# Kernel tuning notes

Hardware: AMD Instinct MI355X
Metric: run time of the kernel (lower is better)

Reference implementation:

```python
import jax, jax.numpy as jnp
import numpy as np

USER_NUM, ITEM_NUM, EMB, R = 8192, 16384, 32, 3

def setup_inputs() -> dict:
    key = jax.random.key(0)
    k1, k2, k3 = jax.random.split(key, 3)
    # Xavier-uniform-like embeddings
    u_lim = (6.0 / (USER_NUM + EMB)) ** 0.5
    i_lim = (6.0 / (ITEM_NUM + EMB)) ** 0.5
    user_emb = jax.random.uniform(k1, (USER_NUM, EMB), jnp.float32, -u_lim, u_lim)
    item_emb = jax.random.uniform(k2, (ITEM_NUM, EMB), jnp.float32, -i_lim, i_lim)
    # Densified normalized link-propagation matrix (user x item).
    # Scale ~1/item_num so repeated propagation stays numerically tame,
    # mimicking the degree-normalized product in __init__.
    sparse_norm = jax.random.uniform(k3, (USER_NUM, ITEM_NUM), jnp.float32) * (2.0 / ITEM_NUM)
    return {"user_emb": user_emb, "item_emb": item_emb, "sparse_norm": sparse_norm}

def reference(user_emb, item_emb, sparse_norm):
    # LinkProp forward (t == 0.0 branch): r rounds of cross propagation,
    # then mean over the (r+1) layer outputs. Running sums avoid stacking.
    u_k, i_k = user_emb, item_emb
    u_sum, i_sum = user_emb, item_emb
    for _ in range(R):
        u_next = sparse_norm @ i_k          # [U, d]
        i_next = sparse_norm.T @ u_k        # [I, d]
        u_sum = u_sum + u_next
        i_sum = i_sum + i_next
        u_k, i_k = u_next, i_next
    inv = 1.0 / (R + 1)
    return (u_sum * inv, i_sum * inv)
```

## Files before the change

kernel.cpp:

```cpp
#include <hip/hip_runtime.h>

#define U_N 8192
#define I_N 16384

typedef float f4 __attribute__((ext_vector_type(4)));
typedef unsigned long long u64;
typedef unsigned char u8;

#if defined(__has_builtin)
#if __has_builtin(__builtin_amdgcn_cvt_pk_fp8_f32)
#define HAS_HW_FP8 1
#endif
#endif
#ifndef HAS_HW_FP8
#define HAS_HW_FP8 0
#endif

__device__ __forceinline__ unsigned char f2e4m3_soft(float x) {
  unsigned char sign = (x < 0.f) ? 0x80 : 0x00;
  float ax = fabsf(x);
  unsigned char code;
  if (ax >= 448.f) {
    code = 0x7E;
  } else if (ax < 0.015625f) {
    int q = (int)rintf(ax * 512.f);
    code = (unsigned char)q;
  } else {
    int e; float f = frexpf(ax, &e);
    int q = (int)rintf(f * 16.f);
    if (q == 16) { q = 8; e += 1; }
    code = (unsigned char)(((e + 6) << 3) | (q - 8));
  }
  return sign | code;
}

__device__ __forceinline__ unsigned char q8(float x) {
#if HAS_HW_FP8
  return (unsigned char)(__builtin_amdgcn_cvt_pk_fp8_f32(x, 0.f, 0, false) & 0xff);
#else
  return f2e4m3_soft(x);
#endif
}

__device__ __forceinline__ unsigned int pack4_fp8(float a, float b, float c, float d) {
#if HAS_HW_FP8
  int v = __builtin_amdgcn_cvt_pk_fp8_f32(a, b, 0, false);
  v = __builtin_amdgcn_cvt_pk_fp8_f32(c, d, v, true);
  return (unsigned int)v;
#else
  return (unsigned)f2e4m3_soft(a) | ((unsigned)f2e4m3_soft(b) << 8) |
         ((unsigned)f2e4m3_soft(c) << 16) | ((unsigned)f2e4m3_soft(d) << 24);
#endif
}

#define SCALE_S   131072.f
#define SCALE_V0  512.f
#define SCALE_VK  65536.f

__global__ __launch_bounds__(256)
void convert_kernel(const float* __restrict__ Sf,
                    const float* __restrict__ u0,
                    const float* __restrict__ i0,
                    u8* __restrict__ S8,
                    u8* __restrict__ S8T,
                    u8* __restrict__ wT0,
                    u8* __restrict__ vT0)
{
  const int tid = threadIdx.x;
  const int bid = blockIdx.x;
  if (bid < 1024) {
    const int idx = bid * 256 + tid;
    wT0[(size_t)(idx & 31) * U_N + (idx >> 5)] = q8(u0[idx] * SCALE_V0);
  } else if (bid < 3072) {
    const int idx = (bid - 1024) * 256 + tid;
    vT0[(size_t)(idx & 31) * I_N + (idx >> 5)] = q8(i0[idx] * SCALE_V0);
  } else {
    __shared__ unsigned char lds[64 * 68];
    const int b = bid - 3072;
    const int tr = b >> 8;
    const int tc = b & 255;
    const int mr = (tid >> 4) << 2;
    const int mc = (tid & 15) << 2;
    const size_t base = ((size_t)tr * 64 + mr) * I_N + (size_t)tc * 64 + mc;
    float fs[4][4];
#pragma unroll
    for (int i = 0; i < 4; ++i) {
      float4 f = *(const float4*)(Sf + base + (size_t)i * I_N);
      fs[i][0] = f.x * SCALE_S; fs[i][1] = f.y * SCALE_S;
      fs[i][2] = f.z * SCALE_S; fs[i][3] = f.w * SCALE_S;
    }
#pragma unroll
    for (int i = 0; i < 4; ++i)
      *(unsigned int*)&S8[base + (size_t)i * I_N] =
          pack4_fp8(fs[i][0], fs[i][1], fs[i][2], fs[i][3]);
#pragma unroll
    for (int j = 0; j < 4; ++j)
      *(unsigned int*)&lds[(mc + j) * 68 + mr] =
          pack4_fp8(fs[0][j], fs[1][j], fs[2][j], fs[3][j]);
    __syncthreads();
    const int c = tid >> 2;
    const int s = (tid & 3) << 4;
    uint4 v;
    v.x = *(const unsigned int*)&lds[c * 68 + s];
    v.y = *(const unsigned int*)&lds[c * 68 + s + 4];
    v.z = *(const unsigned int*)&lds[c * 68 + s + 8];
    v.w = *(const unsigned int*)&lds[c * 68 + s + 12];
    *(uint4*)&S8T[((size_t)tc * 64 + c) * U_N + (size_t)tr * 64 + s] = v;
  }
}

union B16 { uint4 v; long l[2]; };

template <int NE>
__global__ __launch_bounds__(256, 4)
void sweep_kernel(const u8* __restrict__ A, const u8* __restrict__ Bt,
                  float* __restrict__ part, int rg_mask, int rg_shift,
                  int nrows, int kdim, float ds_lo, float ds_hi)
{
  __shared__ u8 smem[NE * 528];
  const int tid = threadIdx.x;
  const int lane = tid & 63, wave = tid >> 6;
  const int m = lane & 15, quad = lane >> 4;
  const int bid = blockIdx.x;
  const int rgroup = bid & rg_mask, ksplit = bid >> rg_shift;
  const int r0 = rgroup * 64 + wave * 16;
  const int kbase = ksplit * 2048;
  f4 acc[NE / 16];
#pragma unroll
  for (int eb = 0; eb < NE / 16; ++eb) acc[eb] = {0.f, 0.f, 0.f, 0.f};

  const u8* arow = A + (size_t)(r0 + m) * kdim;

  for (int ch = 0; ch < 4; ++ch) {
    const int kb = kbase + ch * 512;
#pragma unroll
    for (int it = 0; it < NE / 8; ++it) {
      const int idx = it * 256 + tid;
      const int e = idx >> 5;
      const int o = (idx & 31) * 16;
      *(uint4*)&smem[e * 528 + o] = *(const uint4*)&Bt[(size_t)e * kdim + kb + o];
    }
    __syncthreads();
#pragma unroll
    for (int pr = 0; pr < 8; ++pr) {
      B16 av;
      av.v = *(const uint4*)(arow + kb + pr * 64 + quad * 16);
#pragma unroll
      for (int eb = 0; eb < NE / 16; ++eb) {
        B16 bv;
        bv.v = *(const uint4*)&smem[(m + eb * 16) * 528 + pr * 64 + quad * 16];
        acc[eb] = __builtin_amdgcn_mfma_f32_16x16x32_fp8_fp8(av.l[0], bv.l[0], acc[eb], 0, 0, 0);
        acc[eb] = __builtin_amdgcn_mfma_f32_16x16x32_fp8_fp8(av.l[1], bv.l[1], acc[eb], 0, 0, 0);
      }
    }
    __syncthreads();
  }
  float* dst = part + (size_t)ksplit * ((size_t)nrows * NE);
#pragma unroll
  for (int eb = 0; eb < NE / 16; ++eb) {
    const float ds = (eb < 2) ? ds_lo : ds_hi;
#pragma unroll
    for (int i2 = 0; i2 < 4; ++i2) {
      const int r = r0 + quad * 4 + i2;
      dst[(size_t)r * NE + eb * 16 + m] = acc[eb][i2] * ds;
    }
  }
}

__global__ __launch_bounds__(256)
void reduce_uA(const float* __restrict__ u_part, const float* __restrict__ u0,
               float* __restrict__ acc_u, u8* __restrict__ wT64)
{
  const int gid = blockIdx.x * 256 + threadIdx.x;
  float s = 0.f;
#pragma unroll
  for (int sp = 0; sp < 8; ++sp) s += u_part[(size_t)sp * (U_N * 32) + gid];
  acc_u[gid] = u0[gid] + s;
  wT64[(size_t)(32 + (gid & 31)) * U_N + (gid >> 5)] = q8(s * SCALE_VK);
}

__global__ __launch_bounds__(256)
void reduce_iB(const float* __restrict__ i_part, const float* __restrict__ i0,
               float* __restrict__ acc_i, u8* __restrict__ vT64)
{
  const int gid = blockIdx.x * 256 + threadIdx.x;
  const int c = gid >> 5, e = gid & 31;
  float s1 = 0.f, s2 = 0.f;
#pragma unroll
  for (int sp = 0; sp < 4; ++sp) {
    s1 += i_part[(size_t)sp * (I_N * 64) + (size_t)c * 64 + e];
    s2 += i_part[(size_t)sp * (I_N * 64) + (size_t)c * 64 + 32 + e];
  }
  acc_i[gid] = i0[gid] + s1 + s2;
  vT64[(size_t)e * I_N + c]        = q8(s1 * SCALE_VK);
  vT64[(size_t)(32 + e) * I_N + c] = q8(s2 * SCALE_VK);
}

__global__ __launch_bounds__(256)
void reduce_uC(const float* __restrict__ u_part, const float* __restrict__ acc_u,
               float* __restrict__ out_u, u8* __restrict__ wT2)
{
  const int gid = blockIdx.x * 256 + threadIdx.x;
  const int r = gid >> 5, e = gid & 31;
  float s2 = 0.f, s3 = 0.f;
#pragma unroll
  for (int sp = 0; sp < 8; ++sp) {
    s2 += u_part[(size_t)sp * (U_N * 64) + (size_t)r * 64 + e];
    s3 += u_part[(size_t)sp * (U_N * 64) + (size_t)r * 64 + 32 + e];
  }
  out_u[gid] = (acc_u[gid] + s2 + s3) * 0.25f;
  wT2[(size_t)e * U_N + r] = q8(s2 * SCALE_VK);
}

__global__ __launch_bounds__(256)
void reduce_iD(const float* __restrict__ i_part, const float* __restrict__ acc_i,
               float* __restrict__ out_i)
{
  const int gid = blockIdx.x * 256 + threadIdx.x;
  float s = 0.f;
#pragma unroll
  for (int sp = 0; sp < 4; ++sp) s += i_part[(size_t)sp * (I_N * 32) + gid];
  out_i[gid] = (acc_i[gid] + s) * 0.25f;
}

__global__ __launch_bounds__(256, 4)
void pass_fallback(const float* __restrict__ Sf,
                   const u8* __restrict__ vT,
                   const u8* __restrict__ wT,
                   float* __restrict__ u_part,
                   float* __restrict__ i_part,
                   float descale)
{
  __shared__ unsigned char smem[16896];
  const int tid = threadIdx.x;
  const int lane = tid & 63;
  const int wave = tid >> 6;
  const int m = lane & 15;
  const int quad = lane >> 4;
  const int bid = blockIdx.x;

  if (bid < 1024) {
    const int rg = bid & 127, ks = bid >> 7;
    const int r0 = rg * 64 + wave * 16;
    const int cbase = ks * 2048;
    f4 acc0 = {0.f, 0.f, 0.f, 0.f};
    f4 acc1 = {0.f, 0.f, 0.f, 0.f};
    for (int ch = 0; ch < 4; ++ch) {
      const int cb = cbase + ch * 512;
#pragma unroll
      for (int it = 0; it < 4; ++it) {
        const int idx = it * 256 + tid;
        const int e = idx >> 5;
        const int o = (idx & 31) * 16;
        *(uint4*)&smem[e * 528 + o] = *(const uint4*)&vT[(size_t)e * I_N + cb + o];
      }
      __syncthreads();
#pragma unroll
      for (int kk = 0; kk < 512; kk += 32) {
        const float* p = Sf + (size_t)(r0 + m) * I_N + cb + kk + quad * 8;
        u64 av = 0;
#pragma unroll
        for (int j = 0; j < 8; ++j) av |= (u64)q8(p[j] * SCALE_S) << (8 * j);
        const long a = (long)av;
        const long b0 = *(const long*)&smem[m * 528 + kk + quad * 8];
        const long b1 = *(const long*)&smem[(m + 16) * 528 + kk + quad * 8];
        acc0 = __builtin_amdgcn_mfma_f32_16x16x32_fp8_fp8(a, b0, acc0, 0, 0, 0);
        acc1 = __builtin_amdgcn_mfma_f32_16x16x32_fp8_fp8(a, b1, acc1, 0, 0, 0);
      }
      __syncthreads();
    }
    float* dst = u_part + (size_t)ks * (U_N * 32);
#pragma unroll
    for (int i2 = 0; i2 < 4; ++i2) {
      const int r = r0 + quad * 4 + i2;
      dst[r * 32 + m]      = acc0[i2] * descale;
      dst[r * 32 + 16 + m] = acc1[i2] * descale;
    }
  } else {
    const int b = bid - 1024;
    const int cg = b & 255, rs = b >> 8;
    const int c0 = cg * 64;
    const int rbase = rs * 2048;
    const int cw = wave * 16;
    unsigned char* stile = smem;
    unsigned char* wlds  = smem + 9216;
    f4 acc0 = {0.f, 0.f, 0.f, 0.f};
    f4 acc1 = {0.f, 0.f, 0.f, 0.f};
    for (int ch = 0; ch < 16; ++ch) {
      const int rb = rbase + ch * 128;
#pragma unroll
      for (int it = 0; it < 4; ++it) {
        const int idx = it * 256 + tid;
        const int rr = idx >> 3;
        const int o = (idx & 7) * 8;
        const float* p = Sf + (size_t)(rb + rr) * I_N + c0 + o;
        u64 v = 0;
#pragma unroll
        for (int j = 0; j < 8; ++j) v |= (u64)q8(p[j] * SCALE_S) << (8 * j);
        *(u64*)&stile[rr * 72 + o] = v;
      }
      {
        const int e = tid >> 3;
        const int o = (tid & 7) * 16;
        *(uint4*)&wlds[e * 144 + o] = *(const uint4*)&wT[(size_t)e * U_N + rb + o];
      }
      __syncthreads();
#pragma unroll
      for (int kk = 0; kk < 128; kk += 32) {
        u64 av = 0;
#pragma unroll
        for (int j = 0; j < 8; ++j)
          av |= (u64)stile[(kk + quad * 8 + j) * 72 + cw + m] << (8 * j);
        const long b0 = *(const long*)&wlds[m * 144 + kk + quad * 8];
        const long b1 = *(const long*)&wlds[(m + 16) * 144 + kk + quad * 8];
        acc0 = __builtin_amdgcn_mfma_f32_16x16x32_fp8_fp8((long)av, b0, acc0, 0, 0, 0);
        acc1 = __builtin_amdgcn_mfma_f32_16x16x32_fp8_fp8((long)av, b1, acc1, 0, 0, 0);
      }
      __syncthreads();
    }
    float* dst = i_part + (size_t)rs * (I_N * 32);
#pragma unroll
    for (int i2 = 0; i2 < 4; ++i2) {
      const int c = c0 + cw + quad * 4 + i2;
      dst[c * 32 + m]      = acc0[i2] * descale;
      dst[c * 32 + 16 + m] = acc1[i2] * descale;
    }
  }
}

__global__ __launch_bounds__(256)
void reduce_fallback(const float* __restrict__ u_part, const float* __restrict__ i_part,
                     const float* __restrict__ u0, const float* __restrict__ i0,
                     float* __restrict__ acc_u, float* __restrict__ acc_i,
                     u8* __restrict__ wT, u8* __restrict__ vT,
                     float* __restrict__ out_u, float* __restrict__ out_i,
                     int round)
{
  const int gid = blockIdx.x * 256 + threadIdx.x;
  if (gid < U_N * 32) {
    float s = 0.f;
#pragma unroll
    for (int sp = 0; sp < 8; ++sp) s += u_part[(size_t)sp * (U_N * 32) + gid];
    if (round == 1)      acc_u[gid] = u0[gid] + s;
    else if (round == 2) acc_u[gid] += s;
    else                 out_u[gid] = (acc_u[gid] + s) * 0.25f;
    if (round < 3) wT[(gid & 31) * U_N + (gid >> 5)] = q8(s * SCALE_VK);
  } else {
    const int g = gid - U_N * 32;
    float s = 0.f;
#pragma unroll
    for (int sp = 0; sp < 4; ++sp) s += i_part[(size_t)sp * (I_N * 32) + g];
    if (round == 1)      acc_i[g] = i0[g] + s;
    else if (round == 2) acc_i[g] += s;
    else                 out_i[g] = (acc_i[g] + s) * 0.25f;
    if (round < 3) vT[(g & 31) * I_N + (g >> 5)] = q8(s * SCALE_VK);
  }
}

extern "C" void kernel_launch(void* const* d_in, const int* in_sizes, int n_in,
                              void* d_out, int out_size, void* d_ws, size_t ws_size,
                              hipStream_t stream) {
  const float* u0 = (const float*)d_in[0];
  const float* i0 = (const float*)d_in[1];
  const float* Sf = (const float*)d_in[2];
  float* out_u = (float*)d_out;
  float* out_i = out_u + U_N * 32;
  u8* ws = (u8*)d_ws;

  const size_t S8B = (size_t)U_N * I_N;
  const size_t FULL_BYTES = 2 * S8B
      + (size_t)8 * U_N * 64 * 4 + (size_t)4 * I_N * 64 * 4
      + (size_t)U_N * 32 * 4 + (size_t)I_N * 32 * 4
      + (size_t)64 * U_N + (size_t)64 * I_N
      + (size_t)32 * I_N + (size_t)32 * U_N;
  const bool f8 = ws_size >= FULL_BYTES;

  const float dsA = 1.f / (SCALE_S * SCALE_V0);
  const float dsk = 1.f / (SCALE_S * SCALE_VK);

  if (f8) {
    u8* S8  = ws;
    u8* S8T = ws + S8B;
    float* u_part = (float*)(ws + 2 * S8B);
    float* i_part = u_part + (size_t)8 * U_N * 64;
    float* acc_u  = i_part + (size_t)4 * I_N * 64;
    float* acc_i  = acc_u + U_N * 32;
    u8* wT64 = (u8*)(acc_i + I_N * 32);
    u8* vT64 = wT64 + (size_t)64 * U_N;
    u8* vT0  = vT64 + (size_t)64 * I_N;
    u8* wT2  = vT0 + (size_t)32 * I_N;

    convert_kernel<<<35840, 256, 0, stream>>>(Sf, u0, i0, S8, S8T, wT64, vT0);

    sweep_kernel<32><<<1024, 256, 0, stream>>>(S8, vT0, u_part, 127, 7,
                                               U_N, I_N, dsA, dsA);
    reduce_uA<<<1024, 256, 0, stream>>>(u_part, u0, acc_u, wT64);
    sweep_kernel<64><<<1024, 256, 0, stream>>>(S8T, wT64, i_part, 255, 8,
                                               I_N, U_N, dsA, dsk);
    reduce_iB<<<2048, 256, 0, stream>>>(i_part, i0, acc_i, vT64);
    sweep_kernel<64><<<1024, 256, 0, stream>>>(S8, vT64, u_part, 127, 7,
                                               U_N, I_N, dsk, dsk);
    reduce_uC<<<1024, 256, 0, stream>>>(u_part, acc_u, out_u, wT2);
    sweep_kernel<32><<<1024, 256, 0, stream>>>(S8T, wT2, i_part, 255, 8,
                                               I_N, U_N, dsk, dsk);
    reduce_iD<<<2048, 256, 0, stream>>>(i_part, acc_i, out_i);
  } else {
    float* u_part = (float*)ws;
    float* i_part = u_part + 8 * U_N * 32;
    float* acc_u  = i_part + 4 * I_N * 32;
    float* acc_i  = acc_u + U_N * 32;
    u8* wT = (u8*)(acc_i + I_N * 32);
    u8* vT = wT + 32 * U_N;

    convert_kernel<<<3072, 256, 0, stream>>>(Sf, u0, i0, nullptr, nullptr, wT, vT);
    for (int round = 1; round <= 3; ++round) {
      const float ds = (round == 1) ? dsA : dsk;
      pass_fallback<<<2048, 256, 0, stream>>>(Sf, vT, wT, u_part, i_part, ds);
      reduce_fallback<<<3072, 256, 0, stream>>>(u_part, i_part, u0, i0, acc_u, acc_i,
                                                wT, vT, out_u, out_i, round);
    }
  }
}
```

Measured before the change: 921.6 us.

## Enlarge transpose tiles in fp8 conversion and stage A rows through LDS in sweep

The conversion kernel now handles 128x128 tiles per block instead of 64x64, so each block does more work and the transposed S8T stores become 16-byte rows over longer 128-byte runs, with far fewer blocks launched. The sweep kernel now loads the A-matrix chunk cooperatively into LDS with coalesced 16-byte loads instead of each lane reading its own row directly from global memory. It also halves the K chunk to 256 so A and B fit together in LDS. This adds twice as many barriers per block and more LDS use, which may reduce occupancy.

Result: slower. 1.051 ms (+14.0%).

```diff
diff --git a/kernel.cpp b/kernel.cpp
--- a/kernel.cpp
+++ b/kernel.cpp
@@ -75,37 +75,42 @@
     const int idx = (bid - 1024) * 256 + tid;
     vT0[(size_t)(idx & 31) * I_N + (idx >> 5)] = q8(i0[idx] * SCALE_V0);
   } else {
-    __shared__ unsigned char lds[64 * 68];
+    __shared__ u8 lds_t[128 * 132];
     const int b = bid - 3072;
-    const int tr = b >> 8;
-    const int tc = b & 255;
-    const int mr = (tid >> 4) << 2;
-    const int mc = (tid & 15) << 2;
-    const size_t base = ((size_t)tr * 64 + mr) * I_N + (size_t)tc * 64 + mc;
-    float fs[4][4];
-#pragma unroll
-    for (int i = 0; i < 4; ++i) {
-      float4 f = *(const float4*)(Sf + base + (size_t)i * I_N);
-      fs[i][0] = f.x * SCALE_S; fs[i][1] = f.y * SCALE_S;
-      fs[i][2] = f.z * SCALE_S; fs[i][3] = f.w * SCALE_S;
-    }
-#pragma unroll
-    for (int i = 0; i < 4; ++i)
-      *(unsigned int*)&S8[base + (size_t)i * I_N] =
-          pack4_fp8(fs[i][0], fs[i][1], fs[i][2], fs[i][3]);
-#pragma unroll
-    for (int j = 0; j < 4; ++j)
-      *(unsigned int*)&lds[(mc + j) * 68 + mr] =
-          pack4_fp8(fs[0][j], fs[1][j], fs[2][j], fs[3][j]);
+    const int tr = b >> 7;
+    const int tc = b & 127;
+    const int cg = tid & 31;
+    const int rg = tid >> 5;
+    const size_t rowbase = (size_t)tr * 128;
+    const size_t colbase = (size_t)tc * 128;
+#pragma unroll
+    for (int b4 = 0; b4 < 4; ++b4) {
+      const int R = rg + b4 * 8;
+      const size_t base = (rowbase + 4 * R) * I_N + colbase + cg * 4;
+      float fs[4][4];
+#pragma unroll
+      for (int i = 0; i < 4; ++i) {
+        float4 f = *(const float4*)(Sf + base + (size_t)i * I_N);
+        fs[i][0] = f.x * SCALE_S; fs[i][1] = f.y * SCALE_S;
+        fs[i][2] = f.z * SCALE_S; fs[i][3] = f.w * SCALE_S;
+      }
+#pragma unroll
+      for (int i = 0; i < 4; ++i)
+        *(unsigned int*)&S8[base + (size_t)i * I_N] =
+            pack4_fp8(fs[i][0], fs[i][1], fs[i][2], fs[i][3]);
+#pragma unroll
+      for (int j = 0; j < 4; ++j)
+        *(unsigned int*)&lds_t[(cg * 4 + j) * 132 + 4 * R] =
+            pack4_fp8(fs[0][j], fs[1][j], fs[2][j], fs[3][j]);
+    }
     __syncthreads();
-    const int c = tid >> 2;
-    const int s = (tid & 3) << 4;
-    uint4 v;
-    v.x = *(const unsigned int*)&lds[c * 68 + s];
-    v.y = *(const unsigned int*)&lds[c * 68 + s + 4];
-    v.z = *(const unsigned int*)&lds[c * 68 + s + 8];
-    v.w = *(const unsigned int*)&lds[c * 68 + s + 12];
-    *(uint4*)&S8T[((size_t)tc * 64 + c) * U_N + (size_t)tr * 64 + s] = v;
+    const int k = tid & 7;
+#pragma unroll
+    for (int j = 0; j < 4; ++j) {
+      const int col = j * 32 + (tid >> 3);
+      uint4 v = *(const uint4*)&lds_t[col * 132 + k * 16];
+      *(uint4*)&S8T[(colbase + col) * U_N + rowbase + k * 16] = v;
+    }
   }
 }
 
@@ -117,38 +122,49 @@
                   float* __restrict__ part, int rg_mask, int rg_shift,
                   int nrows, int kdim, float ds_lo, float ds_hi)
 {
-  __shared__ u8 smem[NE * 528];
+  __shared__ u8 lds[(64 + NE) * 264];
+  u8* a_lds = lds;
+  u8* b_lds = lds + 64 * 264;
   const int tid = threadIdx.x;
   const int lane = tid & 63, wave = tid >> 6;
   const int m = lane & 15, quad = lane >> 4;
   const int bid = blockIdx.x;
   const int rgroup = bid & rg_mask, ksplit = bid >> rg_shift;
-  const int r0 = rgroup * 64 + wave * 16;
+  const int r0b = rgroup * 64;
   const int kbase = ksplit * 2048;
   f4 acc[NE / 16];
 #pragma unroll
   for (int eb = 0; eb < NE / 16; ++eb) acc[eb] = {0.f, 0.f, 0.f, 0.f};
 
-  const u8* arow = A + (size_t)(r0 + m) * kdim;
-
-  for (int ch = 0; ch < 4; ++ch) {
-    const int kb = kbase + ch * 512;
-#pragma unroll
-    for (int it = 0; it < NE / 8; ++it) {
+  const int arow = (wave * 16 + m) * 264;
+
+  for (int ch = 0; ch < 8; ++ch) {
+    const int kb = kbase + ch * 256;
+#pragma unroll
+    for (int it = 0; it < 4; ++it) {
       const int idx = it * 256 + tid;
-      const int e = idx >> 5;
-      const int o = (idx & 31) * 16;
-      *(uint4*)&smem[e * 528 + o] = *(const uint4*)&Bt[(size_t)e * kdim + kb + o];
+      const int r = idx >> 4;
+      const int o = (idx & 15) * 16;
+      *(uint4*)&a_lds[r * 264 + o] =
+          *(const uint4*)&A[(size_t)(r0b + r) * kdim + kb + o];
+    }
+#pragma unroll
+    for (int it = 0; it < NE / 16; ++it) {
+      const int idx = it * 256 + tid;
+      const int e = idx >> 4;
+      const int o = (idx & 15) * 16;
+      *(uint4*)&b_lds[e * 264 + o] =
+          *(const uint4*)&Bt[(size_t)e * kdim + kb + o];
     }
     __syncthreads();
 #pragma unroll
-    for (int pr = 0; pr < 8; ++pr) {
+    for (int pr = 0; pr < 4; ++pr) {
       B16 av;
-      av.v = *(const uint4*)(arow + kb + pr * 64 + quad * 16);
+      av.v = *(const uint4*)&a_lds[arow + pr * 64 + quad * 16];
 #pragma unroll
       for (int eb = 0; eb < NE / 16; ++eb) {
         B16 bv;
-        bv.v = *(const uint4*)&smem[(m + eb * 16) * 528 + pr * 64 + quad * 16];
+        bv.v = *(const uint4*)&b_lds[(m + eb * 16) * 264 + pr * 64 + quad * 16];
         acc[eb] = __builtin_amdgcn_mfma_f32_16x16x32_fp8_fp8(av.l[0], bv.l[0], acc[eb], 0, 0, 0);
         acc[eb] = __builtin_amdgcn_mfma_f32_16x16x32_fp8_fp8(av.l[1], bv.l[1], acc[eb], 0, 0, 0);
       }
@@ -161,7 +177,7 @@
     const float ds = (eb < 2) ? ds_lo : ds_hi;
 #pragma unroll
     for (int i2 = 0; i2 < 4; ++i2) {
-      const int r = r0 + quad * 4 + i2;
+      const int r = r0b + wave * 16 + quad * 4 + i2;
       dst[(size_t)r * NE + eb * 16 + m] = acc[eb][i2] * ds;
     }
   }
@@ -390,7 +406,7 @@
     u8* vT0  = vT64 + (size_t)64 * I_N;
     u8* wT2  = vT0 + (size_t)32 * I_N;
 
-    convert_kernel<<<35840, 256, 0, stream>>>(Sf, u0, i0, S8, S8T, wT64, vT0);
+    convert_kernel<<<3072 + 8192, 256, 0, stream>>>(Sf, u0, i0, S8, S8T, wT64, vT0);
 
     sweep_kernel<32><<<1024, 256, 0, stream>>>(S8, vT0, u_part, 127, 7,
                                                U_N, I_N, dsA, dsA);
```
